# Kernel tuning notes

Measured on AMD Instinct MI355X. Metric: run time of the kernel, lower is better.

Reference implementation:

```python
import jax, jax.numpy as jnp
import numpy as np

C = 256
NUM_HEADS = 8
FFN_HIDDEN = C * 2  # ffn_expand=2
EPS = 1e-5


def setup_inputs() -> dict:
    key = jax.random.key(0)
    ks = jax.random.split(key, 12)
    B, H, W = 16, 64, 64
    s = 0.02
    return {
        "optical": jax.random.normal(ks[0], (B, C, H, W), jnp.float32),
        "sar": jax.random.normal(ks[1], (B, C, H, W), jnp.float32),
        "g_opt": jnp.ones((C,), jnp.float32),
        "b_opt": jnp.zeros((C,), jnp.float32),
        "g_sar": jnp.ones((C,), jnp.float32),
        "b_sar": jnp.zeros((C,), jnp.float32),
        "Wq": jax.random.normal(ks[2], (C, C), jnp.float32) * s,
        "Wk": jax.random.normal(ks[3], (C, C), jnp.float32) * s,
        "Wv": jax.random.normal(ks[4], (C, C), jnp.float32) * s,
        "Wo": jax.random.normal(ks[5], (C, C), jnp.float32) * s,
        "g_ffn": jnp.ones((C,), jnp.float32),
        "b_ffn": jnp.zeros((C,), jnp.float32),
        "W1": jax.random.normal(ks[6], (2 * FFN_HIDDEN, C), jnp.float32) * s,
        "b1": jnp.zeros((2 * FFN_HIDDEN,), jnp.float32),
        "W2": jax.random.normal(ks[7], (C, FFN_HIDDEN), jnp.float32) * s,
        "b2": jnp.zeros((C,), jnp.float32),
    }


def _ln(x, g, b):
    # LayerNorm over channel axis of (B, C, H, W), biased variance, eps=1e-5
    mu = jnp.mean(x, axis=1, keepdims=True)
    var = jnp.mean(jnp.square(x - mu), axis=1, keepdims=True)
    xn = (x - mu) * jax.lax.rsqrt(var + EPS)
    return xn * g[None, :, None, None] + b[None, :, None, None]


def _proj(x, Wmat):
    # 1x1 conv == channel matmul
    return jnp.einsum('oc,bchw->bohw', Wmat, x)


def reference(optical, sar, g_opt, b_opt, g_sar, b_sar, Wq, Wk, Wv, Wo,
              g_ffn, b_ffn, W1, b1, W2, b2):
    B, Cc, H, W = optical.shape
    hc = Cc // NUM_HEADS
    L = H * W
    scale = hc ** -0.5

    opt_n = _ln(optical, g_opt, b_opt)
    sar_n = _ln(sar, g_sar, b_sar)

    # channel (transposed) attention: contraction over spatial L
    q = _proj(opt_n, Wq).reshape(B, NUM_HEADS, hc, L)
    k = _proj(sar_n, Wk).reshape(B, NUM_HEADS, hc, L)
    v = _proj(sar_n, Wv).reshape(B, NUM_HEADS, hc, L)
    A = jax.nn.softmax(jnp.einsum('bhcl,bhdl->bhcd', q, k) * scale, axis=-1)
    attn = jnp.einsum('bhcd,bhdl->bhcl', A, v).reshape(B, Cc, H, W)
    x = optical + _proj(attn, Wo)

    # SimpleGate FFN
    h = _ln(x, g_ffn, b_ffn)
    h = _proj(h, W1) + b1[None, :, None, None]
    h1, h2 = jnp.split(h, 2, axis=1)
    h = _proj(h1 * h2, W2) + b2[None, :, None, None]
    return x + h
```

## Files before the change

### kernel.cpp

```cpp
#include <hip/hip_runtime.h>
#include <hip/hip_bf16.h>

typedef __bf16 bf16;
typedef __attribute__((ext_vector_type(8))) __bf16 bf16x8;
typedef __attribute__((ext_vector_type(4))) __bf16 bf16x4;
typedef __attribute__((ext_vector_type(4))) float f32x4;
typedef __attribute__((ext_vector_type(16))) float f32x16;

#define LSP 4096
#define CCH 256

__device__ __forceinline__ void gl2lds16(const bf16* g, bf16* l) {
  __builtin_amdgcn_global_load_lds(
      (const __attribute__((address_space(1))) unsigned int*)g,
      (__attribute__((address_space(3))) unsigned int*)l, 16, 0, 0);
}

__device__ __forceinline__ f32x4 mfma16(bf16x8 a, bf16x8 b, f32x4 c) {
  return __builtin_amdgcn_mfma_f32_16x16x32_bf16(a, b, c, 0, 0, 0);
}
__device__ __forceinline__ f32x16 mfma32(bf16x8 a, bf16x8 b, f32x16 c) {
  return __builtin_amdgcn_mfma_f32_32x32x16_bf16(a, b, c, 0, 0, 0);
}

__global__ __launch_bounds__(256) void cvt_w_kernel(
    const float* __restrict__ wq, const float* __restrict__ wk,
    const float* __restrict__ wv, const float* __restrict__ wo,
    const float* __restrict__ w1, const float* __restrict__ w2,
    const float* __restrict__ gff, bf16* __restrict__ out) {
  int e = blockIdx.x * 256 + threadIdx.x;
  if (e < 65536)        { out[e] = (bf16)wq[e]; }
  else if (e < 131072)  { out[e] = (bf16)wk[e - 65536]; }
  else if (e < 196608)  {
    int e2 = e - 131072;
    int och = e2 >> 8, cin = e2 & 255;
    out[131072 + cin * 256 + och] = (bf16)wv[e2];
  }
  else if (e < 262144)  { out[e] = (bf16)wo[e - 196608]; }
  else if (e < 524288)  {
    int e2 = e - 262144;
    int m = e2 >> 8, k = e2 & 255;
    int mp = (m < 512) ? (2 * m) : (2 * (m - 512) + 1);
    out[262144 + mp * 256 + k] = (bf16)(w1[e2] * gff[k]);
  }
  else                  { out[e] = (bf16)w2[e - 524288]; }
}

__global__ __launch_bounds__(256) void w1vec_kernel(
    const float* __restrict__ w1, const float* __restrict__ b1,
    const float* __restrict__ gff, const float* __restrict__ bff,
    float* __restrict__ cvec) {
  int m = blockIdx.x * 256 + threadIdx.x;
  const float* row = w1 + (size_t)m * 256;
  float sb = 0.f, sg = 0.f;
  #pragma unroll 8
  for (int c = 0; c < 256; c += 4) {
    f32x4 w = *(const f32x4*)&row[c];
    f32x4 g = *(const f32x4*)&gff[c];
    f32x4 bb = *(const f32x4*)&bff[c];
    #pragma unroll
    for (int j = 0; j < 4; ++j) { sb += w[j] * bb[j]; sg += w[j] * g[j]; }
  }
  if (m < 512) {
    cvec[m] = sb + b1[m];
    cvec[512 + m] = sg;
  } else {
    cvec[512 + m] = sb + b1[m];
    cvec[1024 + m] = sg;
  }
}

template <int DUAL>
__global__ __launch_bounds__(256) void ln_tile_kernel(
    const float* __restrict__ x, const float* __restrict__ gam,
    const float* __restrict__ bet, bf16* __restrict__ out_cl,
    bf16* __restrict__ out_lc) {
  const int l0 = blockIdx.x * 64;
  const int b  = blockIdx.y;
  const int tid = threadIdx.x;
  __shared__ bf16 Tt[256 * 64];
  __shared__ float red[2][16][64];
  __shared__ float mu_s[64], rs_s[64];

  const float* px = x + (size_t)b * CCH * LSP + l0;
  const int colq = (tid & 15) * 4;
  f32x4 s = {0.f, 0.f, 0.f, 0.f}, q = {0.f, 0.f, 0.f, 0.f};
  #pragma unroll
  for (int it = 0; it < 16; ++it) {
    int c = it * 16 + (tid >> 4);
    f32x4 v = *(const f32x4*)&px[(size_t)c * LSP + colq];
    s += v;
    q += v * v;
    bf16x4 h;
    #pragma unroll
    for (int j = 0; j < 4; ++j) h[j] = (bf16)v[j];
    int colp = colq ^ (((c >> 3) & 7) << 3);
    *(bf16x4*)&Tt[c * 64 + colp] = h;
  }
  #pragma unroll
  for (int j = 0; j < 4; ++j) {
    red[0][tid >> 4][colq + j] = s[j];
    red[1][tid >> 4][colq + j] = q[j];
  }
  __syncthreads();
  if (tid < 64) {
    float S = 0.f, Q = 0.f;
    #pragma unroll
    for (int k = 0; k < 16; ++k) { S += red[0][k][tid]; Q += red[1][k][tid]; }
    float m = S * (1.f / 256.f);
    mu_s[tid] = m;
    rs_s[tid] = rsqrtf(Q * (1.f / 256.f) - m * m + 1e-5f);
  }
  __syncthreads();

  #pragma unroll
  for (int it = 0; it < 8; ++it) {
    int ch = it * 256 + tid;
    int c = ch >> 3, col8 = (ch & 7) * 8;
    int colp = col8 ^ (((c >> 3) & 7) << 3);
    bf16x8 h = *(const bf16x8*)&Tt[c * 64 + colp];
    f32x4 m0 = *(const f32x4*)&mu_s[col8];
    f32x4 m1 = *(const f32x4*)&mu_s[col8 + 4];
    f32x4 r0 = *(const f32x4*)&rs_s[col8];
    f32x4 r1 = *(const f32x4*)&rs_s[col8 + 4];
    float g = gam[c], be = bet[c];
    bf16x8 o;
    #pragma unroll
    for (int j = 0; j < 4; ++j) {
      o[j]     = (bf16)(((float)h[j] - m0[j]) * r0[j] * g + be);
      o[4 + j] = (bf16)(((float)h[4 + j] - m1[j]) * r1[j] * g + be);
    }
    *(bf16x8*)&out_cl[((size_t)b * CCH + c) * LSP + l0 + col8] = o;
  }

  if constexpr (DUAL) {
    #pragma unroll
    for (int it = 0; it < 8; ++it) {
      int ch = it * 256 + tid;
      int l = ch >> 5, cch = ch & 31;
      int c0 = cch * 8;
      int lp = l ^ ((cch & 7) << 3);
      float mu = mu_s[l], rs = rs_s[l];
      f32x4 g0 = *(const f32x4*)&gam[c0];
      f32x4 g1 = *(const f32x4*)&gam[c0 + 4];
      f32x4 b0 = *(const f32x4*)&bet[c0];
      f32x4 b1 = *(const f32x4*)&bet[c0 + 4];
      bf16x8 o;
      #pragma unroll
      for (int j = 0; j < 4; ++j) {
        float h0 = (float)Tt[(c0 + j) * 64 + lp];
        float h1 = (float)Tt[(c0 + 4 + j) * 64 + lp];
        o[j]     = (bf16)((h0 - mu) * rs * g0[j] + b0[j]);
        o[4 + j] = (bf16)((h1 - mu) * rs * g1[j] + b1[j]);
      }
      *(bf16x8*)&out_lc[((size_t)b * LSP + l0 + l) * CCH + c0] = o;
    }
  }
}

__global__ __launch_bounds__(256) void gram_kernel(
    const bf16* __restrict__ sar_cl, const bf16* __restrict__ opt_cl,
    float* __restrict__ part) {
  const int tile = blockIdx.x, chunk = blockIdx.y, b = blockIdx.z;
  const int tid = threadIdx.x, lane = tid & 63, w = tid >> 6;
  const int j0 = (tile >> 1) * 128 + (w >> 1) * 64;
  const int i0 = (tile & 1) * 128 + (w & 1) * 64;
  const int l0 = chunk * 1024;
  const bf16* sj = sar_cl + ((size_t)b * CCH + j0 + (lane & 31)) * LSP + l0;
  const bf16* oi = opt_cl + ((size_t)b * CCH + i0 + (lane & 31)) * LSP + l0;
  f32x16 acc[2][2];
  #pragma unroll
  for (int mt = 0; mt < 2; ++mt)
    #pragma unroll
    for (int nt = 0; nt < 2; ++nt)
      #pragma unroll
      for (int r = 0; r < 16; ++r) acc[mt][nt][r] = 0.f;
  #pragma unroll 4
  for (int ks = 0; ks < 64; ++ks) {
    int lofs = ks * 16 + (lane >> 5) * 8;
    bf16x8 a0 = *(const bf16x8*)&sj[lofs];
    bf16x8 a1 = *(const bf16x8*)&sj[32 * LSP + lofs];
    bf16x8 b0 = *(const bf16x8*)&oi[lofs];
    bf16x8 b1 = *(const bf16x8*)&oi[32 * LSP + lofs];
    acc[0][0] = mfma32(a0, b0, acc[0][0]);
    acc[0][1] = mfma32(a0, b1, acc[0][1]);
    acc[1][0] = mfma32(a1, b0, acc[1][0]);
    acc[1][1] = mfma32(a1, b1, acc[1][1]);
  }
  float* op = part + ((size_t)chunk * 16 + b) * 65536;
  #pragma unroll
  for (int mt = 0; mt < 2; ++mt)
    #pragma unroll
    for (int nt = 0; nt < 2; ++nt)
      #pragma unroll
      for (int r = 0; r < 16; ++r) {
        int row = j0 + mt * 32 + (r & 3) + 8 * (r >> 2) + 4 * (lane >> 5);
        int col = i0 + nt * 32 + (lane & 31);
        op[(size_t)row * 256 + col] = acc[mt][nt][r];
      }
}

__global__ __launch_bounds__(256) void greduce_kernel(
    const float* __restrict__ part, bf16* __restrict__ G2) {
  size_t e = ((size_t)blockIdx.x * 256 + threadIdx.x) * 8;
  float a[8];
  #pragma unroll
  for (int i = 0; i < 8; ++i) a[i] = 0.f;
  #pragma unroll
  for (int ch = 0; ch < 4; ++ch) {
    f32x4 p0 = *(const f32x4*)&part[ch * 1048576ull + e];
    f32x4 p1 = *(const f32x4*)&part[ch * 1048576ull + e + 4];
    #pragma unroll
    for (int i = 0; i < 4; ++i) { a[i] += p0[i]; a[4 + i] += p1[i]; }
  }
  bf16x8 o;
  #pragma unroll
  for (int i = 0; i < 8; ++i) o[i] = (bf16)a[i];
  *(bf16x8*)&G2[e] = o;
}

__global__ __launch_bounds__(256) void fold2_kernel(
    const bf16* __restrict__ G2, const bf16* __restrict__ Wq,
    const bf16* __restrict__ Wk, const bf16* __restrict__ WvT,
    bf16* __restrict__ UT) {
  const int bh = blockIdx.x;
  const int b = bh >> 3, h = bh & 7;
  const int tid = threadIdx.x, lane = tid & 63, w = tid >> 6;
  __shared__ bf16 M1[32 * 256];
  __shared__ float Sp[4][1024];
  __shared__ float S[1024];
  __shared__ bf16 P[1024];

  const bf16* gq = Wq + (size_t)(h * 32) * 256;
  const bf16* g2b = G2 + (size_t)b * 65536;
  #pragma unroll
  for (int mt = 0; mt < 2; ++mt)
    #pragma unroll
    for (int nt = 0; nt < 4; ++nt) {
      f32x4 acc = {0.f, 0.f, 0.f, 0.f};
      #pragma unroll
      for (int ks = 0; ks < 8; ++ks) {
        bf16x8 a = *(const bf16x8*)&gq[(size_t)(mt * 16 + (lane & 15)) * 256 +
                                       ks * 32 + (lane >> 4) * 8];
        bf16x8 bb = *(const bf16x8*)&g2b[
            (size_t)(w * 64 + nt * 16 + (lane & 15)) * 256 + ks * 32 +
            (lane >> 4) * 8];
        acc = mfma16(a, bb, acc);
      }
      #pragma unroll
      for (int r = 0; r < 4; ++r)
        M1[(mt * 16 + (lane >> 4) * 4 + r) * 256 + w * 64 + nt * 16 +
           (lane & 15)] = (bf16)acc[r];
    }
  __syncthreads();

  const bf16* gk = Wk + (size_t)(h * 32) * 256;
  #pragma unroll
  for (int mt = 0; mt < 2; ++mt)
    #pragma unroll
    for (int dt = 0; dt < 2; ++dt) {
      f32x4 acc = {0.f, 0.f, 0.f, 0.f};
      #pragma unroll
      for (int kk = 0; kk < 2; ++kk) {
        bf16x8 a = *(const bf16x8*)&M1[(mt * 16 + (lane & 15)) * 256 + w * 64 +
                                       kk * 32 + (lane >> 4) * 8];
        bf16x8 bb = *(const bf16x8*)&gk[(size_t)(dt * 16 + (lane & 15)) * 256 +
                                        w * 64 + kk * 32 + (lane >> 4) * 8];
        acc = mfma16(a, bb, acc);
      }
      #pragma unroll
      for (int r = 0; r < 4; ++r)
        Sp[w][(mt * 16 + (lane >> 4) * 4 + r) * 32 + dt * 16 + (lane & 15)] =
            acc[r];
    }
  __syncthreads();
  #pragma unroll
  for (int i = 0; i < 4; ++i) {
    int e = tid + 256 * i;
    S[e] = (Sp[0][e] + Sp[1][e] + Sp[2][e] + Sp[3][e]) * 0.17677669529663687f;
  }
  __syncthreads();
  if (tid < 32) {
    float m = -1e30f;
    #pragma unroll
    for (int d = 0; d < 32; ++d) m = fmaxf(m, S[tid * 32 + d]);
    float sum = 0.f;
    float ex[32];
    #pragma unroll
    for (int d = 0; d < 32; ++d) {
      ex[d] = __expf(S[tid * 32 + d] - m);
      sum += ex[d];
    }
    float inv = 1.f / sum;
    #pragma unroll
    for (int d = 0; d < 32; ++d) P[tid * 32 + d] = (bf16)(ex[d] * inv);
  }
  __syncthreads();

  bf16x8 bfrag[2];
  #pragma unroll
  for (int ct = 0; ct < 2; ++ct)
    bfrag[ct] =
        *(const bf16x8*)&P[(ct * 16 + (lane & 15)) * 32 + (lane >> 4) * 8];
  bf16* outb = UT + (size_t)b * 65536 + h * 32;
  #pragma unroll
  for (int t = 0; t < 4; ++t) {
    int cin16 = w * 64 + t * 16;
    bf16x8 afrag = *(const bf16x8*)&WvT[(size_t)(cin16 + (lane & 15)) * 256 +
                                        h * 32 + (lane >> 4) * 8];
    #pragma unroll
    for (int ct = 0; ct < 2; ++ct) {
      f32x4 acc = {0.f, 0.f, 0.f, 0.f};
      acc = mfma16(afrag, bfrag[ct], acc);
      int c = ct * 16 + (lane & 15);
      int cinr = cin16 + (lane >> 4) * 4;
      #pragma unroll
      for (int r = 0; r < 4; ++r)
        outb[(size_t)(cinr + r) * 256 + c] = (bf16)acc[r];
    }
  }
}

__global__ __launch_bounds__(256) void wfold_kernel(
    const bf16* __restrict__ Aw, const bf16* __restrict__ Bx,
    bf16* __restrict__ outp) {
  const int tid = threadIdx.x;
  const int lane = tid & 63;
  const int wave = tid >> 6;
  const int wr = wave >> 1, wc = wave & 1;
  const int l0 = blockIdx.x * 128;
  const int m0 = blockIdx.y * 128;
  const int b  = blockIdx.z;
  constexpr int NB = 4096;
  __shared__ bf16 smem[4 * NB];
  bf16* As = smem;
  bf16* Bs = smem + 2 * NB;
  const bf16* Ag = Aw + (size_t)m0 * 256;
  const bf16* Bg = Bx + ((size_t)b * 256 + l0) * 256;
  auto stage = [&](int buf, int k0) {
    #pragma unroll
    for (int i = 0; i < 2; ++i) {
      int ch = i * 256 + tid;
      int r  = ch >> 2;
      int c8 = (ch & 3) * 8;
      gl2lds16(Ag + (size_t)r * 256 + k0 + c8, As + buf * NB + ch * 8);
      gl2lds16(Bg + (size_t)r * 256 + k0 + c8, Bs + buf * NB + ch * 8);
    }
  };
  f32x4 acc[4][4];
  #pragma unroll
  for (int mi = 0; mi < 4; ++mi)
    #pragma unroll
    for (int ni = 0; ni < 4; ++ni)
      #pragma unroll
      for (int r = 0; r < 4; ++r) acc[mi][ni][r] = 0.f;
  stage(0, 0);
  for (int kt = 0; kt < 8; ++kt) {
    __syncthreads();
    if (kt + 1 < 8) stage((kt + 1) & 1, (kt + 1) * 32);
    const bf16* Ab = As + (kt & 1) * NB;
    const bf16* Bb = Bs + (kt & 1) * NB;
    bf16x8 af[4], bfr[4];
    #pragma unroll
    for (int mi = 0; mi < 4; ++mi)
      af[mi] = *(const bf16x8*)&Ab[(wr * 64 + mi * 16 + (lane & 15)) * 32 +
                                   (lane >> 4) * 8];
    #pragma unroll
    for (int ni = 0; ni < 4; ++ni)
      bfr[ni] = *(const bf16x8*)&Bb[(wc * 64 + ni * 16 + (lane & 15)) * 32 +
                                    (lane >> 4) * 8];
    #pragma unroll
    for (int mi = 0; mi < 4; ++mi)
      #pragma unroll
      for (int ni = 0; ni < 4; ++ni)
        acc[mi][ni] = mfma16(af[mi], bfr[ni], acc[mi][ni]);
  }
  const int mq = m0 + wr * 64 + (lane >> 4) * 4;
  const int lq = l0 + wc * 64 + (lane & 15);
  #pragma unroll
  for (int mi = 0; mi < 4; ++mi)
    #pragma unroll
    for (int ni = 0; ni < 4; ++ni) {
      int l = lq + ni * 16, mb = mq + mi * 16;
      #pragma unroll
      for (int r = 0; r < 4; ++r)
        outp[((size_t)b * 256 + mb + r) * 256 + l] = (bf16)acc[mi][ni][r];
    }
}

__global__ __launch_bounds__(256) void xgemm_stats_kernel(
    const bf16* __restrict__ Wfold, const bf16* __restrict__ sar_lc,
    const float* __restrict__ optical, bf16* __restrict__ xout,
    float* __restrict__ stats) {
  const int tid = threadIdx.x, lane = tid & 63, w = tid >> 6;
  const int l0 = blockIdx.x * 64;
  const int b  = blockIdx.y;
  __shared__ __align__(16) char smem[43520];
  bf16* X = (bf16*)smem;
  float* red = (float*)(smem + 40960);

  const bf16* Ag = Wfold + (size_t)b * 65536;
  const bf16* Bg = sar_lc + ((size_t)b * LSP + l0) * CCH;

  auto stage = [&](int buf, int k0) {
    bf16* As = (bf16*)(smem + buf * 16384);
    bf16* Bs = (bf16*)(smem + 32768 + buf * 4096);
    #pragma unroll
    for (int i = 0; i < 4; ++i) {
      int ch = i * 256 + tid;
      int r = ch >> 2, c8 = (ch & 3) * 8;
      gl2lds16(Ag + (size_t)r * 256 + k0 + c8, &As[ch * 8]);
    }
    {
      int r = tid >> 2, c8 = (tid & 3) * 8;
      gl2lds16(Bg + (size_t)r * 256 + k0 + c8, &Bs[tid * 8]);
    }
  };

  f32x4 acc[4][4];
  #pragma unroll
  for (int mi = 0; mi < 4; ++mi)
    #pragma unroll
    for (int ni = 0; ni < 4; ++ni)
      #pragma unroll
      for (int r = 0; r < 4; ++r) acc[mi][ni][r] = 0.f;

  stage(0, 0);
  for (int kt = 0; kt < 8; ++kt) {
    __syncthreads();
    if (kt < 7) stage((kt + 1) & 1, (kt + 1) * 32);
    const bf16* Ab = (const bf16*)(smem + (kt & 1) * 16384);
    const bf16* Bb = (const bf16*)(smem + 32768 + (kt & 1) * 4096);
    bf16x8 af[4], bfr[4];
    #pragma unroll
    for (int mi = 0; mi < 4; ++mi)
      af[mi] = *(const bf16x8*)&Ab[(w * 64 + mi * 16 + (lane & 15)) * 32 +
                                   (lane >> 4) * 8];
    #pragma unroll
    for (int ni = 0; ni < 4; ++ni)
      bfr[ni] = *(const bf16x8*)&Bb[(ni * 16 + (lane & 15)) * 32 +
                                    (lane >> 4) * 8];
    #pragma unroll
    for (int mi = 0; mi < 4; ++mi)
      #pragma unroll
      for (int ni = 0; ni < 4; ++ni)
        acc[mi][ni] = mfma16(af[mi], bfr[ni], acc[mi][ni]);
  }
  __syncthreads();

  const int cb = w * 64 + (lane >> 4) * 4;
  const int lb = lane & 15;
  float s[4], q[4];
  #pragma unroll
  for (int ni = 0; ni < 4; ++ni) { s[ni] = 0.f; q[ni] = 0.f; }
  #pragma unroll
  for (int mi = 0; mi < 4; ++mi)
    #pragma unroll
    for (int ni = 0; ni < 4; ++ni) {
      int c = cb + mi * 16, ll = lb + ni * 16;
      bf16x4 hx;
      #pragma unroll
      for (int r = 0; r < 4; ++r) {
        float v = acc[mi][ni][r] +
                  optical[((size_t)b * CCH + c + r) * LSP + l0 + ll];
        s[ni] += v; q[ni] += v * v;
        hx[r] = (bf16)v;
      }
      *(bf16x4*)&X[ll * 260 + c] = hx;
    }
  #pragma unroll
  for (int ni = 0; ni < 4; ++ni) {
    s[ni] += __shfl_xor(s[ni], 16);
    s[ni] += __shfl_xor(s[ni], 32);
    q[ni] += __shfl_xor(q[ni], 16);
    q[ni] += __shfl_xor(q[ni], 32);
  }
  if ((lane >> 4) == 0) {
    #pragma unroll
    for (int ni = 0; ni < 4; ++ni) {
      red[(0 * 4 + w) * 64 + ni * 16 + lb] = s[ni];
      red[(4 + w) * 64 + ni * 16 + lb] = q[ni];
    }
  }
  __syncthreads();
  if (tid < 64) {
    float S4 = red[0 * 64 + tid] + red[1 * 64 + tid] + red[2 * 64 + tid] +
               red[3 * 64 + tid];
    float Q4 = red[4 * 64 + tid] + red[5 * 64 + tid] + red[6 * 64 + tid] +
               red[7 * 64 + tid];
    float m = S4 * (1.f / 256.f);
    float rs = rsqrtf(Q4 * (1.f / 256.f) - m * m + 1e-5f);
    float* st = stats + ((size_t)b * LSP + l0 + tid) * 2;
    st[0] = m;
    st[1] = rs;
  }
  __syncthreads();
  #pragma unroll
  for (int it = 0; it < 8; ++it) {
    int cid = it * 256 + tid;
    int l = cid >> 5, c0 = (cid & 31) * 8;
    bf16x8 v = *(const bf16x8*)&X[l * 260 + c0];
    *(bf16x8*)&xout[((size_t)b * LSP + l0 + l) * CCH + c0] = v;
  }
}

template <int KEL, int MODE>
__global__ __launch_bounds__(512, 4) void ffn_gemm_kernel(
    const bf16* __restrict__ Aw, const bf16* __restrict__ Bx,
    void* __restrict__ outp, const bf16* __restrict__ resb,
    const float* __restrict__ bias, const float* __restrict__ stats) {
  __shared__ __align__(16) char smem[49152];
  const int tid = threadIdx.x;
  const int lane = tid & 63;
  const int wave = tid >> 6;
  const int wr = wave >> 2;
  const int wc = wave & 3;
  const int l0 = blockIdx.x * 128;
  const int m0 = blockIdx.y * 256;
  const int b  = blockIdx.z;

  const bf16* Ag = Aw + (size_t)m0 * KEL;
  const bf16* Bg = Bx + ((size_t)b * LSP + l0) * KEL;

  auto stage = [&](int buf, int kt) {
    char* la = smem + (buf << 14);
    char* lb2 = smem + 32768 + (buf << 13);
    #pragma unroll
    for (int i = 0; i < 2; ++i) {
      int qi = i * 512 + tid;
      int r = qi >> 2, c = qi & 3;
      int gc = c ^ ((r >> 1) & 3);
      gl2lds16(Ag + (size_t)r * KEL + kt * 32 + gc * 8,
               (bf16*)(la + qi * 16));
    }
    {
      int r = tid >> 2, c = tid & 3;
      int gc = c ^ ((r >> 1) & 3);
      gl2lds16(Bg + (size_t)r * KEL + kt * 32 + gc * 8,
               (bf16*)(lb2 + tid * 16));
    }
  };

  f32x4 acc[8][2];
  #pragma unroll
  for (int mi = 0; mi < 8; ++mi)
    #pragma unroll
    for (int ni = 0; ni < 2; ++ni)
      #pragma unroll
      for (int r = 0; r < 4; ++r) acc[mi][ni][r] = 0.f;

  constexpr int NK = KEL / 32;
  stage(0, 0);
  for (int kt = 0; kt < NK; ++kt) {
    __syncthreads();
    if (kt + 1 < NK) stage((kt + 1) & 1, kt + 1);
    const char* Ab = smem + ((kt & 1) << 14);
    const char* Bb = smem + 32768 + ((kt & 1) << 13);
    bf16x8 af[8], bf2[2];
    #pragma unroll
    for (int mi = 0; mi < 8; ++mi) {
      int row = wr * 128 + mi * 16 + (lane & 15);
      int c = (lane >> 4) ^ ((row >> 1) & 3);
      af[mi] = *(const bf16x8*)(Ab + row * 64 + c * 16);
    }
    #pragma unroll
    for (int ni = 0; ni < 2; ++ni) {
      int row = wc * 32 + ni * 16 + (lane & 15);
      int c = (lane >> 4) ^ ((row >> 1) & 3);
      bf2[ni] = *(const bf16x8*)(Bb + row * 64 + c * 16);
    }
    #pragma unroll
    for (int mi = 0; mi < 8; ++mi)
      #pragma unroll
      for (int ni = 0; ni < 2; ++ni)
        acc[mi][ni] = mfma16(af[mi], bf2[ni], acc[mi][ni]);
  }
  __syncthreads();

  const int qq = lane >> 4;
  if constexpr (MODE == 0) {
    bf16* g_lds = (bf16*)smem;
    const int lq = wc * 32 + (lane & 15);
    const float* stb = stats + ((size_t)b * LSP + l0) * 2;
    float muv[2], rsv[2];
    #pragma unroll
    for (int ni = 0; ni < 2; ++ni) {
      int l = lq + ni * 16;
      muv[ni] = stb[l * 2];
      rsv[ni] = stb[l * 2 + 1];
    }
    #pragma unroll
    for (int mi = 0; mi < 8; ++mi) {
      int a0 = wr * 64 + mi * 8 + qq * 2;
      int ag = (m0 >> 1) + a0;
      float be1a = bias[ag],        ga1a = bias[512 + ag];
      float be2a = bias[1024 + ag], ga2a = bias[1536 + ag];
      float be1b = bias[ag + 1],        ga1b = bias[512 + ag + 1];
      float be2b = bias[1024 + ag + 1], ga2b = bias[1536 + ag + 1];
      #pragma unroll
      for (int ni = 0; ni < 2; ++ni) {
        int l = lq + ni * 16;
        float mrs = muv[ni] * rsv[ni];
        float h1a = rsv[ni] * acc[mi][ni][0] + be1a - mrs * ga1a;
        float h2a = rsv[ni] * acc[mi][ni][1] + be2a - mrs * ga2a;
        float h1b = rsv[ni] * acc[mi][ni][2] + be1b - mrs * ga1b;
        float h2b = rsv[ni] * acc[mi][ni][3] + be2b - mrs * ga2b;
        bf16 gv0 = (bf16)(h1a * h2a), gv1 = (bf16)(h1b * h2b);
        unsigned u = ((unsigned)*(unsigned short*)&gv1 << 16) |
                     (unsigned)*(unsigned short*)&gv0;
        *(unsigned*)&g_lds[l * 136 + a0] = u;
      }
    }
    __syncthreads();
    bf16* out = (bf16*)outp;
    const int gy = blockIdx.y * 128;
    #pragma unroll
    for (int it = 0; it < 4; ++it) {
      int cid = it * 512 + tid;
      int l = cid >> 4, ch = cid & 15;
      bf16x8 v = *(const bf16x8*)&g_lds[l * 136 + ch * 8];
      *(bf16x8*)&out[((size_t)b * LSP + l0 + l) * 512 + gy + ch * 8] = v;
    }
  } else {
    float* lds_f = (float*)smem;
    float* out = (float*)outp;
    const int lq = wc * 32 + (lane & 15);
    #pragma unroll
    for (int round = 0; round < 4; ++round) {
      if (wr == (round >> 1)) {
        #pragma unroll
        for (int mj = 0; mj < 4; ++mj) {
          int mi = (round & 1) * 4 + mj;
          int c0r = mj * 16 + qq * 4;
          int cg = round * 64 + c0r;
          f32x4 b4 = *(const f32x4*)&bias[cg];
          #pragma unroll
          for (int ni = 0; ni < 2; ++ni) {
            int l = lq + ni * 16;
            bf16x4 xr4 = *(const bf16x4*)&resb[((size_t)b * LSP + l0 + l) *
                                                   CCH + cg];
            #pragma unroll
            for (int r = 0; r < 4; ++r)
              lds_f[(c0r + r) * 132 + l] =
                  acc[mi][ni][r] + b4[r] + (float)xr4[r];
          }
        }
      }
      __syncthreads();
      #pragma unroll
      for (int it = 0; it < 4; ++it) {
        int cid = it * 512 + tid;
        int c = cid >> 5, lch = cid & 31;
        f32x4 v = *(const f32x4*)&lds_f[c * 132 + lch * 4];
        *(f32x4*)&out[((size_t)b * CCH + round * 64 + c) * LSP + l0 +
                      lch * 4] = v;
      }
      __syncthreads();
    }
  }
}

extern "C" void kernel_launch(void* const* d_in, const int* in_sizes, int n_in,
                              void* d_out, int out_size, void* d_ws,
                              size_t ws_size, hipStream_t stream) {
  const float* optical = (const float*)d_in[0];
  const float* sar     = (const float*)d_in[1];
  const float* g_opt   = (const float*)d_in[2];
  const float* b_opt   = (const float*)d_in[3];
  const float* g_sar   = (const float*)d_in[4];
  const float* b_sar   = (const float*)d_in[5];
  const float* Wq      = (const float*)d_in[6];
  const float* Wk      = (const float*)d_in[7];
  const float* Wv      = (const float*)d_in[8];
  const float* Wo      = (const float*)d_in[9];
  const float* g_ffn   = (const float*)d_in[10];
  const float* b_ffn   = (const float*)d_in[11];
  const float* W1      = (const float*)d_in[12];
  const float* b1      = (const float*)d_in[13];
  const float* W2      = (const float*)d_in[14];
  const float* b2      = (const float*)d_in[15];

  char* ws = (char*)d_ws;
  bf16* wbf  = (bf16*)ws;
  bf16* Wqb  = wbf;
  bf16* Wkb  = wbf + 65536;
  bf16* WvTb = wbf + 131072;
  bf16* Wob  = wbf + 196608;
  bf16* W1b  = wbf + 262144;
  bf16* W2b  = wbf + 524288;

  size_t off = 2ull * 1024 * 1024;
  const size_t T16 = 16ull * LSP * CCH * 2;
  bf16* opt_ncl = (bf16*)(ws + off); off += T16;
  bf16* sar_ncl = (bf16*)(ws + off); off += T16;
  bf16* sar_nlc = (bf16*)(ws + off); off += T16;
  bf16* xb      = (bf16*)(ws + off); off += T16;
  float* stats  = (float*)(ws + off); off += 1ull * 1024 * 1024;
  float* cvec   = (float*)(ws + off); off += 64 * 1024;
  float* Gpart  = (float*)(ws + off); off += 16ull * 1024 * 1024;
  bf16* G2b     = (bf16*)(ws + off); off += 4ull * 1024 * 1024;
  bf16* UTb     = (bf16*)(ws + off); off += 2ull * 1024 * 1024;
  bf16* Wfoldb  = (bf16*)(ws + off); off += 2ull * 1024 * 1024;
  bf16* gbuf = opt_ncl;

  dim3 blk(256);
  cvt_w_kernel<<<2560, blk, 0, stream>>>(Wq, Wk, Wv, Wo, W1, W2, g_ffn, wbf);
  w1vec_kernel<<<4, blk, 0, stream>>>(W1, b1, g_ffn, b_ffn, cvec);
  ln_tile_kernel<0><<<dim3(64, 16), blk, 0, stream>>>(optical, g_opt, b_opt,
                                                      opt_ncl, nullptr);
  ln_tile_kernel<1><<<dim3(64, 16), blk, 0, stream>>>(sar, g_sar, b_sar,
                                                      sar_ncl, sar_nlc);
  gram_kernel<<<dim3(4, 4, 16), blk, 0, stream>>>(sar_ncl, opt_ncl, Gpart);
  greduce_kernel<<<512, blk, 0, stream>>>(Gpart, G2b);
  fold2_kernel<<<128, blk, 0, stream>>>(G2b, Wqb, Wkb, WvTb, UTb);
  wfold_kernel<<<dim3(2, 2, 16), blk, 0, stream>>>(Wob, UTb, Wfoldb);
  xgemm_stats_kernel<<<dim3(64, 16), blk, 0, stream>>>(Wfoldb, sar_nlc,
                                                       optical, xb, stats);
  ffn_gemm_kernel<256, 0><<<dim3(32, 4, 16), dim3(512), 0, stream>>>(
      W1b, xb, gbuf, nullptr, cvec, stats);
  ffn_gemm_kernel<512, 1><<<dim3(32, 1, 16), dim3(512), 0, stream>>>(
      W2b, gbuf, (float*)d_out, xb, b2, nullptr);
}
```

Baseline: 259.5 us.

## Fuse FFN up and down GEMMs into one kernel and read optical residual as bf16

Replaces the two FFN GEMM launches with one fused kernel. Each 64-column tile keeps x in LDS, computes the gated hidden activations chunk by chunk into LDS, and accumulates the W2 output in registers, so the 1024-wide intermediate never goes to global memory. Separately, the optical LN kernel now also writes a raw bf16 channel-last copy of optical, and the residual add reads it coalesced instead of gathering strided fp32. The trade-offs are that W1/W2 fragments are loaded straight from global/L2 without LDS staging, and the residual is rounded to bf16, which costs some precision.

```diff
diff --git a/kernel.cpp b/kernel.cpp
--- a/kernel.cpp
+++ b/kernel.cpp
@@ -70,11 +70,11 @@
   }
 }
 
-template <int DUAL>
+template <int DUAL, int RAW>
 __global__ __launch_bounds__(256) void ln_tile_kernel(
     const float* __restrict__ x, const float* __restrict__ gam,
     const float* __restrict__ bet, bf16* __restrict__ out_cl,
-    bf16* __restrict__ out_lc) {
+    bf16* __restrict__ out_lc, bf16* __restrict__ out_raw) {
   const int l0 = blockIdx.x * 64;
   const int b  = blockIdx.y;
   const int tid = threadIdx.x;
@@ -154,6 +154,22 @@
         o[4 + j] = (bf16)((h1 - mu) * rs * g1[j] + b1[j]);
       }
       *(bf16x8*)&out_lc[((size_t)b * LSP + l0 + l) * CCH + c0] = o;
+    }
+  }
+  if constexpr (RAW) {
+    #pragma unroll
+    for (int it = 0; it < 8; ++it) {
+      int ch = it * 256 + tid;
+      int l = ch >> 5, cch = ch & 31;
+      int c0 = cch * 8;
+      int lp = l ^ ((cch & 7) << 3);
+      bf16x8 o;
+      #pragma unroll
+      for (int j = 0; j < 4; ++j) {
+        o[j]     = Tt[(c0 + j) * 64 + lp];
+        o[4 + j] = Tt[(c0 + 4 + j) * 64 + lp];
+      }
+      *(bf16x8*)&out_raw[((size_t)b * LSP + l0 + l) * CCH + c0] = o;
     }
   }
 }
@@ -390,7 +406,7 @@
 
 __global__ __launch_bounds__(256) void xgemm_stats_kernel(
     const bf16* __restrict__ Wfold, const bf16* __restrict__ sar_lc,
-    const float* __restrict__ optical, bf16* __restrict__ xout,
+    const bf16* __restrict__ opt_raw, bf16* __restrict__ xout,
     float* __restrict__ stats) {
   const int tid = threadIdx.x, lane = tid & 63, w = tid >> 6;
   const int l0 = blockIdx.x * 64;
@@ -458,11 +474,11 @@
     #pragma unroll
     for (int ni = 0; ni < 4; ++ni) {
       int c = cb + mi * 16, ll = lb + ni * 16;
+      bf16x4 o4 = *(const bf16x4*)&opt_raw[((size_t)b * LSP + l0 + ll) * CCH + c];
       bf16x4 hx;
       #pragma unroll
       for (int r = 0; r < 4; ++r) {
-        float v = acc[mi][ni][r] +
-                  optical[((size_t)b * CCH + c + r) * LSP + l0 + ll];
+        float v = acc[mi][ni][r] + (float)o4[r];
         s[ni] += v; q[ni] += v * v;
         hx[r] = (bf16)v;
       }
@@ -504,159 +520,137 @@
   }
 }
 
-template <int KEL, int MODE>
-__global__ __launch_bounds__(512, 4) void ffn_gemm_kernel(
-    const bf16* __restrict__ Aw, const bf16* __restrict__ Bx,
-    void* __restrict__ outp, const bf16* __restrict__ resb,
-    const float* __restrict__ bias, const float* __restrict__ stats) {
-  __shared__ __align__(16) char smem[49152];
+__global__ __launch_bounds__(512, 4) void ffn_fused_kernel(
+    const bf16* __restrict__ W1i, const bf16* __restrict__ W2,
+    const bf16* __restrict__ xb, float* __restrict__ out,
+    const float* __restrict__ cvec, const float* __restrict__ b2v,
+    const float* __restrict__ stats) {
+  __shared__ __align__(16) char smem[51200];
+  bf16* xs = (bf16*)smem;
   const int tid = threadIdx.x;
   const int lane = tid & 63;
-  const int wave = tid >> 6;
-  const int wr = wave >> 2;
-  const int wc = wave & 3;
-  const int l0 = blockIdx.x * 128;
-  const int m0 = blockIdx.y * 256;
-  const int b  = blockIdx.z;
-
-  const bf16* Ag = Aw + (size_t)m0 * KEL;
-  const bf16* Bg = Bx + ((size_t)b * LSP + l0) * KEL;
-
-  auto stage = [&](int buf, int kt) {
-    char* la = smem + (buf << 14);
-    char* lb2 = smem + 32768 + (buf << 13);
-    #pragma unroll
-    for (int i = 0; i < 2; ++i) {
-      int qi = i * 512 + tid;
-      int r = qi >> 2, c = qi & 3;
-      int gc = c ^ ((r >> 1) & 3);
-      gl2lds16(Ag + (size_t)r * KEL + kt * 32 + gc * 8,
-               (bf16*)(la + qi * 16));
+  const int w = tid >> 6;
+  const int l0 = blockIdx.x * 64;
+  const int b  = blockIdx.y;
+  const int qq = lane >> 4;
+  const int lr = lane & 15;
+
+  const bf16* xg = xb + ((size_t)b * LSP + l0) * CCH;
+  #pragma unroll
+  for (int i = 0; i < 4; ++i) {
+    int qi = i * 512 + tid;
+    int r = qi >> 5, c = qi & 31;
+    int gc = c ^ (r & 31);
+    gl2lds16(xg + (size_t)r * CCH + gc * 8, xs + qi * 8);
+  }
+
+  const float* stb = stats + ((size_t)b * LSP + l0) * 2;
+  float muv[4], rsv[4];
+  #pragma unroll
+  for (int nq = 0; nq < 4; ++nq) {
+    int l = nq * 16 + lr;
+    muv[nq] = stb[l * 2];
+    rsv[nq] = stb[l * 2 + 1];
+  }
+
+  f32x4 acc2[2][4];
+  #pragma unroll
+  for (int mt = 0; mt < 2; ++mt)
+    #pragma unroll
+    for (int nq = 0; nq < 4; ++nq)
+      #pragma unroll
+      for (int r = 0; r < 4; ++r) acc2[mt][nq][r] = 0.f;
+
+  __syncthreads();
+
+  for (int chunk = 0; chunk < 8; ++chunk) {
+    bf16* g2 = (bf16*)(smem + 32768 + (chunk & 1) * 9216);
+
+    f32x4 acc1[4];
+    #pragma unroll
+    for (int nq = 0; nq < 4; ++nq)
+      #pragma unroll
+      for (int r = 0; r < 4; ++r) acc1[nq][r] = 0.f;
+    const bf16* w1p = W1i + (size_t)(chunk * 128 + w * 16 + lr) * CCH;
+    #pragma unroll
+    for (int ks = 0; ks < 8; ++ks) {
+      bf16x8 a = *(const bf16x8*)&w1p[ks * 32 + qq * 8];
+      #pragma unroll
+      for (int nq = 0; nq < 4; ++nq) {
+        int l = nq * 16 + lr;
+        int cc = (ks * 4 + qq) ^ (l & 31);
+        bf16x8 bb = *(const bf16x8*)&xs[l * 256 + cc * 8];
+        acc1[nq] = mfma16(a, bb, acc1[nq]);
+      }
     }
     {
-      int r = tid >> 2, c = tid & 3;
-      int gc = c ^ ((r >> 1) & 3);
-      gl2lds16(Bg + (size_t)r * KEL + kt * 32 + gc * 8,
-               (bf16*)(lb2 + tid * 16));
-    }
-  };
-
-  f32x4 acc[8][2];
-  #pragma unroll
-  for (int mi = 0; mi < 8; ++mi)
-    #pragma unroll
-    for (int ni = 0; ni < 2; ++ni)
-      #pragma unroll
-      for (int r = 0; r < 4; ++r) acc[mi][ni][r] = 0.f;
-
-  constexpr int NK = KEL / 32;
-  stage(0, 0);
-  for (int kt = 0; kt < NK; ++kt) {
-    __syncthreads();
-    if (kt + 1 < NK) stage((kt + 1) & 1, kt + 1);
-    const char* Ab = smem + ((kt & 1) << 14);
-    const char* Bb = smem + 32768 + ((kt & 1) << 13);
-    bf16x8 af[8], bf2[2];
-    #pragma unroll
-    for (int mi = 0; mi < 8; ++mi) {
-      int row = wr * 128 + mi * 16 + (lane & 15);
-      int c = (lane >> 4) ^ ((row >> 1) & 3);
-      af[mi] = *(const bf16x8*)(Ab + row * 64 + c * 16);
-    }
-    #pragma unroll
-    for (int ni = 0; ni < 2; ++ni) {
-      int row = wc * 32 + ni * 16 + (lane & 15);
-      int c = (lane >> 4) ^ ((row >> 1) & 3);
-      bf2[ni] = *(const bf16x8*)(Bb + row * 64 + c * 16);
-    }
-    #pragma unroll
-    for (int mi = 0; mi < 8; ++mi)
-      #pragma unroll
-      for (int ni = 0; ni < 2; ++ni)
-        acc[mi][ni] = mfma16(af[mi], bf2[ni], acc[mi][ni]);
-  }
-  __syncthreads();
-
-  const int qq = lane >> 4;
-  if constexpr (MODE == 0) {
-    bf16* g_lds = (bf16*)smem;
-    const int lq = wc * 32 + (lane & 15);
-    const float* stb = stats + ((size_t)b * LSP + l0) * 2;
-    float muv[2], rsv[2];
-    #pragma unroll
-    for (int ni = 0; ni < 2; ++ni) {
-      int l = lq + ni * 16;
-      muv[ni] = stb[l * 2];
-      rsv[ni] = stb[l * 2 + 1];
-    }
-    #pragma unroll
-    for (int mi = 0; mi < 8; ++mi) {
-      int a0 = wr * 64 + mi * 8 + qq * 2;
-      int ag = (m0 >> 1) + a0;
-      float be1a = bias[ag],        ga1a = bias[512 + ag];
-      float be2a = bias[1024 + ag], ga2a = bias[1536 + ag];
-      float be1b = bias[ag + 1],        ga1b = bias[512 + ag + 1];
-      float be2b = bias[1024 + ag + 1], ga2b = bias[1536 + ag + 1];
-      #pragma unroll
-      for (int ni = 0; ni < 2; ++ni) {
-        int l = lq + ni * 16;
-        float mrs = muv[ni] * rsv[ni];
-        float h1a = rsv[ni] * acc[mi][ni][0] + be1a - mrs * ga1a;
-        float h2a = rsv[ni] * acc[mi][ni][1] + be2a - mrs * ga2a;
-        float h1b = rsv[ni] * acc[mi][ni][2] + be1b - mrs * ga1b;
-        float h2b = rsv[ni] * acc[mi][ni][3] + be2b - mrs * ga2b;
+      int ag = chunk * 64 + w * 8 + qq * 2;
+      float be1a = cvec[ag],        ga1a = cvec[512 + ag];
+      float be2a = cvec[1024 + ag], ga2a = cvec[1536 + ag];
+      float be1b = cvec[ag + 1],        ga1b = cvec[512 + ag + 1];
+      float be2b = cvec[1024 + ag + 1], ga2b = cvec[1536 + ag + 1];
+      int gc0 = w * 8 + qq * 2;
+      #pragma unroll
+      for (int nq = 0; nq < 4; ++nq) {
+        int l = nq * 16 + lr;
+        float mrs = muv[nq] * rsv[nq];
+        float h1a = rsv[nq] * acc1[nq][0] + be1a - mrs * ga1a;
+        float h2a = rsv[nq] * acc1[nq][1] + be2a - mrs * ga2a;
+        float h1b = rsv[nq] * acc1[nq][2] + be1b - mrs * ga1b;
+        float h2b = rsv[nq] * acc1[nq][3] + be2b - mrs * ga2b;
         bf16 gv0 = (bf16)(h1a * h2a), gv1 = (bf16)(h1b * h2b);
         unsigned u = ((unsigned)*(unsigned short*)&gv1 << 16) |
                      (unsigned)*(unsigned short*)&gv0;
-        *(unsigned*)&g_lds[l * 136 + a0] = u;
+        *(unsigned*)&g2[l * 72 + gc0] = u;
       }
     }
     __syncthreads();
-    bf16* out = (bf16*)outp;
-    const int gy = blockIdx.y * 128;
+
+    const bf16* w2p = W2 + (size_t)(w * 32 + lr) * 512 + chunk * 64;
+    #pragma unroll
+    for (int ks2 = 0; ks2 < 2; ++ks2) {
+      bf16x8 a0 = *(const bf16x8*)&w2p[ks2 * 32 + qq * 8];
+      bf16x8 a1 = *(const bf16x8*)&w2p[16 * 512 + ks2 * 32 + qq * 8];
+      #pragma unroll
+      for (int nq = 0; nq < 4; ++nq) {
+        int l = nq * 16 + lr;
+        bf16x8 bb = *(const bf16x8*)&g2[l * 72 + ks2 * 32 + qq * 8];
+        acc2[0][nq] = mfma16(a0, bb, acc2[0][nq]);
+        acc2[1][nq] = mfma16(a1, bb, acc2[1][nq]);
+      }
+    }
+  }
+  __syncthreads();
+
+  float* lds_f = (float*)smem;
+  #pragma unroll
+  for (int h = 0; h < 2; ++h) {
+    if ((w >> 2) == h) {
+      #pragma unroll
+      for (int mt = 0; mt < 2; ++mt) {
+        int cbase = w * 32 + mt * 16 + qq * 4;
+        int crl = cbase - h * 128;
+        f32x4 b4 = *(const f32x4*)&b2v[cbase];
+        #pragma unroll
+        for (int nq = 0; nq < 4; ++nq) {
+          int l = nq * 16 + lr;
+          bf16x4 xr4 = *(const bf16x4*)&xb[((size_t)b * LSP + l0 + l) * CCH +
+                                           cbase];
+          #pragma unroll
+          for (int r = 0; r < 4; ++r)
+            lds_f[(crl + r) * 68 + l] = acc2[mt][nq][r] + b4[r] + (float)xr4[r];
+        }
+      }
+    }
+    __syncthreads();
     #pragma unroll
     for (int it = 0; it < 4; ++it) {
       int cid = it * 512 + tid;
-      int l = cid >> 4, ch = cid & 15;
-      bf16x8 v = *(const bf16x8*)&g_lds[l * 136 + ch * 8];
-      *(bf16x8*)&out[((size_t)b * LSP + l0 + l) * 512 + gy + ch * 8] = v;
-    }
-  } else {
-    float* lds_f = (float*)smem;
-    float* out = (float*)outp;
-    const int lq = wc * 32 + (lane & 15);
-    #pragma unroll
-    for (int round = 0; round < 4; ++round) {
-      if (wr == (round >> 1)) {
-        #pragma unroll
-        for (int mj = 0; mj < 4; ++mj) {
-          int mi = (round & 1) * 4 + mj;
-          int c0r = mj * 16 + qq * 4;
-          int cg = round * 64 + c0r;
-          f32x4 b4 = *(const f32x4*)&bias[cg];
-          #pragma unroll
-          for (int ni = 0; ni < 2; ++ni) {
-            int l = lq + ni * 16;
-            bf16x4 xr4 = *(const bf16x4*)&resb[((size_t)b * LSP + l0 + l) *
-                                                   CCH + cg];
-            #pragma unroll
-            for (int r = 0; r < 4; ++r)
-              lds_f[(c0r + r) * 132 + l] =
-                  acc[mi][ni][r] + b4[r] + (float)xr4[r];
-          }
-        }
-      }
-      __syncthreads();
-      #pragma unroll
-      for (int it = 0; it < 4; ++it) {
-        int cid = it * 512 + tid;
-        int c = cid >> 5, lch = cid & 31;
-        f32x4 v = *(const f32x4*)&lds_f[c * 132 + lch * 4];
-        *(f32x4*)&out[((size_t)b * CCH + round * 64 + c) * LSP + l0 +
-                      lch * 4] = v;
-      }
-      __syncthreads();
-    }
+      int c = cid >> 4, lch = cid & 15;
+      f32x4 v = *(const f32x4*)&lds_f[c * 68 + lch * 4];
+      *(f32x4*)&out[((size_t)b * CCH + h * 128 + c) * LSP + l0 + lch * 4] = v;
+    }
+    __syncthreads();
   }
 }
 
@@ -694,6 +688,7 @@
   bf16* opt_ncl = (bf16*)(ws + off); off += T16;
   bf16* sar_ncl = (bf16*)(ws + off); off += T16;
   bf16* sar_nlc = (bf16*)(ws + off); off += T16;
+  bf16* opt_raw = (bf16*)(ws + off); off += T16;
   bf16* xb      = (bf16*)(ws + off); off += T16;
   float* stats  = (float*)(ws + off); off += 1ull * 1024 * 1024;
   float* cvec   = (float*)(ws + off); off += 64 * 1024;
@@ -701,23 +696,20 @@
   bf16* G2b     = (bf16*)(ws + off); off += 4ull * 1024 * 1024;
   bf16* UTb     = (bf16*)(ws + off); off += 2ull * 1024 * 1024;
   bf16* Wfoldb  = (bf16*)(ws + off); off += 2ull * 1024 * 1024;
-  bf16* gbuf = opt_ncl;
 
   dim3 blk(256);
   cvt_w_kernel<<<2560, blk, 0, stream>>>(Wq, Wk, Wv, Wo, W1, W2, g_ffn, wbf);
   w1vec_kernel<<<4, blk, 0, stream>>>(W1, b1, g_ffn, b_ffn, cvec);
-  ln_tile_kernel<0><<<dim3(64, 16), blk, 0, stream>>>(optical, g_opt, b_opt,
-                                                      opt_ncl, nullptr);
-  ln_tile_kernel<1><<<dim3(64, 16), blk, 0, stream>>>(sar, g_sar, b_sar,
-                                                      sar_ncl, sar_nlc);
+  ln_tile_kernel<0, 1><<<dim3(64, 16), blk, 0, stream>>>(
+      optical, g_opt, b_opt, opt_ncl, nullptr, opt_raw);
+  ln_tile_kernel<1, 0><<<dim3(64, 16), blk, 0, stream>>>(
+      sar, g_sar, b_sar, sar_ncl, sar_nlc, nullptr);
   gram_kernel<<<dim3(4, 4, 16), blk, 0, stream>>>(sar_ncl, opt_ncl, Gpart);
   greduce_kernel<<<512, blk, 0, stream>>>(Gpart, G2b);
   fold2_kernel<<<128, blk, 0, stream>>>(G2b, Wqb, Wkb, WvTb, UTb);
   wfold_kernel<<<dim3(2, 2, 16), blk, 0, stream>>>(Wob, UTb, Wfoldb);
   xgemm_stats_kernel<<<dim3(64, 16), blk, 0, stream>>>(Wfoldb, sar_nlc,
-                                                       optical, xb, stats);
-  ffn_gemm_kernel<256, 0><<<dim3(32, 4, 16), dim3(512), 0, stream>>>(
-      W1b, xb, gbuf, nullptr, cvec, stats);
-  ffn_gemm_kernel<512, 1><<<dim3(32, 1, 16), dim3(512), 0, stream>>>(
-      W2b, gbuf, (float*)d_out, xb, b2, nullptr);
-}
+                                                       opt_raw, xb, stats);
+  ffn_fused_kernel<<<dim3(64, 16), dim3(512), 0, stream>>>(
+      W1b, W2b, xb, (float*)d_out, cvec, b2, stats);
+}
```

New measurement: 296.7 us. 1.14x slower.
